# Kernel tuning notes

Hardware: AMD Instinct MI355X
Metric: run time of the kernel (lower is better)

Reference implementation:

```python
import jax, jax.numpy as jnp
import numpy as np

NU, NV, NF = 100000, 50000, 5000
D = 64
S, EUV = 5, 500000
EUF, EVF, EFU, EFV = 1000000, 500000, 1000000, 500000


def _spmm(rows, cols, vals, x, n_out):
    # COO sparse @ dense: out[r] += v * x[c]
    return jax.ops.segment_sum(vals[:, None] * x[cols], rows, num_segments=n_out)


def setup_inputs() -> dict:
    key = jax.random.key(0)
    ks = iter(jax.random.split(key, 32))
    f32 = jnp.float32
    inp = {
        'x_u': jax.random.normal(next(ks), (NU, D), f32),
        'x_v': jax.random.normal(next(ks), (NV, D), f32),
        'x_f': jax.random.normal(next(ks), (NF, D), f32),
    }
    for w in ['W_u_uv', 'W_v_uv', 'W_f2u', 'W_f2v', 'W_u2f', 'W_v2f']:
        inp[w] = jax.random.normal(next(ks), (D, D), f32) * (1.0 / np.sqrt(D))
    def edges(name, shape, n_row, n_col):
        inp[name + '_rows'] = jax.random.randint(next(ks), shape, 0, n_row, jnp.int32)
        inp[name + '_cols'] = jax.random.randint(next(ks), shape, 0, n_col, jnp.int32)
        inp[name + '_vals'] = jax.random.uniform(next(ks), shape, f32)
    edges('uv', (S, EUV), NU, NV)
    edges('vu', (S, EUV), NV, NU)
    edges('uf', (EUF,), NU, NF)
    edges('vf', (EVF,), NV, NF)
    edges('fu', (EFU,), NF, NU)
    edges('fv', (EFV,), NF, NV)
    return inp


def reference(x_u, x_v, x_f, W_u_uv, W_v_uv, W_f2u, W_f2v, W_u2f, W_v2f,
              uv_rows, uv_cols, uv_vals, vu_rows, vu_cols, vu_vals,
              uf_rows, uf_cols, uf_vals, vf_rows, vf_cols, vf_vals,
              fu_rows, fu_cols, fu_vals, fv_rows, fv_cols, fv_vals):
    nu, nv, nf = x_u.shape[0], x_v.shape[0], x_f.shape[0]
    # dense feature transforms (dropout=0 -> identity)
    u2f = x_u @ W_u2f
    v2f = x_v @ W_v2f
    f2u = x_f @ W_f2u
    f2v = x_f @ W_f2v
    tmp_u = x_u @ W_u_uv
    tmp_v = x_v @ W_v_uv
    # sum over rating supports == one segment_sum over flattened edges
    msg_u = _spmm(uv_rows.reshape(-1), uv_cols.reshape(-1), uv_vals.reshape(-1), tmp_v, nu)
    msg_v = _spmm(vu_rows.reshape(-1), vu_cols.reshape(-1), vu_vals.reshape(-1), tmp_u, nv)
    msg_u = msg_u + _spmm(uf_rows, uf_cols, uf_vals, f2u, nu)
    msg_v = msg_v + _spmm(vf_rows, vf_cols, vf_vals, f2v, nv)
    msg_f = _spmm(fu_rows, fu_cols, fu_vals, u2f, nf) + _spmm(fv_rows, fv_cols, fv_vals, v2f, nf)
    return jax.nn.relu(msg_u), jax.nn.relu(msg_v), jax.nn.relu(msg_f)
```

## Files before the change

### kernel.cpp

```cpp
#include <hip/hip_runtime.h>


#define TDIM 64
#define EPB  4096

struct Rel {
    const int* rows; const int* cols; const float* vals;
    int n, chunk0, boff, shift, srcflag, eoff;
};
struct RelPack { Rel r[6]; };

struct TPack {
    const float* X[3]; const float* W1[3]; const float* W2[3];
    unsigned short* Y1[3]; unsigned short* Y2[3];
    int N[3]; int c0[3];
};

struct FSPack {
    int c0A[3], cntA[3], offA[3];
    int c0B[3], cntB[3], offB[3];
};

struct GatherPack {
    const unsigned* srcA[3]; const unsigned* srcB[3];
    int n0, n1;
};

__device__ __forceinline__ unsigned short f2bf(float f) {
    union { float f; unsigned u; } c; c.f = f;
    unsigned r = c.u + 0x7FFFu + ((c.u >> 16) & 1u);
    return (unsigned short)(r >> 16);
}
__device__ __forceinline__ float bflo(unsigned x) { return __uint_as_float(x << 16); }
__device__ __forceinline__ float bfhi(unsigned x) { return __uint_as_float(x & 0xFFFF0000u); }
__device__ __forceinline__ float pval(unsigned p) {
    return __uint_as_float((p & 0x7FFFu) << 16);
}

__global__ __launch_bounds__(256) void transform_fused_kernel(TPack T)
{
    __shared__ float xsT[64 * 68];
    __shared__ float w1s[64 * 64];
    __shared__ float w2s[64 * 64];

    int t = 0;
    if ((int)blockIdx.x >= T.c0[1]) t = 1;
    if ((int)blockIdx.x >= T.c0[2]) t = 2;
    const float* __restrict__ X  = T.X[t];
    const float* __restrict__ W1 = T.W1[t];
    const float* __restrict__ W2 = T.W2[t];
    unsigned short* __restrict__ Y1 = T.Y1[t];
    unsigned short* __restrict__ Y2 = T.Y2[t];
    const int N    = T.N[t];
    const int row0 = (blockIdx.x - T.c0[t]) * 64;
    const int tid  = threadIdx.x;

    for (int i = tid * 4; i < 4096; i += 256 * 4) {
        *(float4*)&w1s[i] = *(const float4*)&W1[i];
        *(float4*)&w2s[i] = *(const float4*)&W2[i];
    }
    {
        const int r  = tid >> 2;
        const int c0 = (tid & 3) * 16;
        const int gr = row0 + r;
        #pragma unroll
        for (int cc = 0; cc < 16; cc += 4) {
            const int c = c0 + cc;
            float4 v = make_float4(0.f, 0.f, 0.f, 0.f);
            if (gr < N) v = *(const float4*)&X[(size_t)gr * TDIM + c];
            xsT[(c + 0) * 68 + r] = v.x;
            xsT[(c + 1) * 68 + r] = v.y;
            xsT[(c + 2) * 68 + r] = v.z;
            xsT[(c + 3) * 68 + r] = v.w;
        }
    }
    __syncthreads();

    const int tx = tid & 15;
    const int ty = tid >> 4;
    float a1[4][4] = {{0.f}}, a2[4][4] = {{0.f}};

    #pragma unroll 8
    for (int k = 0; k < 64; ++k) {
        const float4 xv = *(const float4*)&xsT[k * 68 + ty * 4];
        const float4 w1 = *(const float4*)&w1s[k * 64 + tx * 4];
        const float4 w2 = *(const float4*)&w2s[k * 64 + tx * 4];
        const float xr[4] = {xv.x, xv.y, xv.z, xv.w};
        const float c1[4] = {w1.x, w1.y, w1.z, w1.w};
        const float c2[4] = {w2.x, w2.y, w2.z, w2.w};
        #pragma unroll
        for (int r = 0; r < 4; ++r)
            #pragma unroll
            for (int c = 0; c < 4; ++c) {
                a1[r][c] = fmaf(xr[r], c1[c], a1[r][c]);
                a2[r][c] = fmaf(xr[r], c2[c], a2[r][c]);
            }
    }
    #pragma unroll
    for (int r = 0; r < 4; ++r) {
        const int gr = row0 + ty * 4 + r;
        if (gr < N) {
            ushort4 o1, o2;
            o1.x = f2bf(a1[r][0]); o1.y = f2bf(a1[r][1]);
            o1.z = f2bf(a1[r][2]); o1.w = f2bf(a1[r][3]);
            o2.x = f2bf(a2[r][0]); o2.y = f2bf(a2[r][1]);
            o2.z = f2bf(a2[r][2]); o2.w = f2bf(a2[r][3]);
            ((ushort4*)Y1)[(size_t)gr * 16 + tx] = o1;
            ((ushort4*)Y2)[(size_t)gr * 16 + tx] = o2;
        }
    }
}

__device__ __forceinline__ int find_rel(const RelPack& P, int chunk) {
    int ri = 0;
    if (chunk >= P.r[1].chunk0) ri = 1;
    if (chunk >= P.r[2].chunk0) ri = 2;
    if (chunk >= P.r[3].chunk0) ri = 3;
    if (chunk >= P.r[4].chunk0) ri = 4;
    if (chunk >= P.r[5].chunk0) ri = 5;
    return ri;
}

__global__ __launch_bounds__(512) void bucketize_cm_kernel(
    RelPack P, uint2* __restrict__ recs, int* __restrict__ localStart,
    int* __restrict__ bucketTotal, int NB)
{
    __shared__ int cnt[1024];
    __shared__ int sh[512];
    __shared__ uint2 stage[EPB];

    const int tid   = threadIdx.x;
    const int chunk = blockIdx.x;
    for (int t = tid; t < NB; t += 512) cnt[t] = 0;
    __syncthreads();

    const int ri = find_rel(P, chunk);
    const Rel M = P.r[ri];
    const int i0    = (chunk - M.chunk0) * EPB;
    const int rbase = M.eoff + i0;
    const int count = min(EPB, M.n - i0);

    const unsigned flag = (unsigned)M.srcflag << 31;
    const int mask = (1 << M.shift) - 1;

    int      m_[EPB / 512];
    unsigned x_[EPB / 512];
    #pragma unroll
    for (int k = 0; k < EPB / 512; ++k) {
        const int i = i0 + tid + k * 512;
        m_[k] = -1;
        if (i < M.n) {
            const int row = M.rows[i];
            const int b   = M.boff + (row >> M.shift);
            m_[k] = (b << 8) | (row & mask);
            x_[k] = (unsigned)M.cols[i] | flag;
            atomicAdd(&cnt[b], 1);
        }
    }
    __syncthreads();

    const int i0b = 2 * tid, i1b = 2 * tid + 1;
    const int v0 = (i0b < NB) ? cnt[i0b] : 0;
    const int v1 = (i1b < NB) ? cnt[i1b] : 0;
    if (v0) atomicAdd(&bucketTotal[i0b], v0);
    if (v1) atomicAdd(&bucketTotal[i1b], v1);
    sh[tid] = v0 + v1;
    __syncthreads();
    for (int off = 1; off < 512; off <<= 1) {
        const int x = (tid >= off) ? sh[tid - off] : 0;
        __syncthreads();
        sh[tid] += x;
        __syncthreads();
    }
    const int base0 = tid ? sh[tid - 1] : 0;

    const size_t lb = (size_t)chunk * (NB + 1);
    if (i0b < NB) localStart[lb + i0b] = base0;
    if (i1b < NB) localStart[lb + i1b] = base0 + v0;
    if (i0b == NB)      localStart[lb + NB] = base0;
    else if (i1b == NB) localStart[lb + NB] = base0 + v0;
    if (i0b < NB) cnt[i0b] = base0;
    if (i1b < NB) cnt[i1b] = base0 + v0;
    __syncthreads();

    #pragma unroll
    for (int k = 0; k < EPB / 512; ++k) {
        if (m_[k] >= 0) {
            const int i   = i0 + tid + k * 512;
            const int bin = m_[k] >> 8;
            const int pos = atomicAdd(&cnt[bin], 1);
            uint2 rec;
            rec.x = x_[k];
            rec.y = ((unsigned)(m_[k] & 255) << 16) | (unsigned)f2bf(M.vals[i]);
            stage[pos] = rec;
        }
    }
    __syncthreads();

    #pragma unroll
    for (int k = 0; k < EPB / 512; ++k) {
        const int j = tid + k * 512;
        if (j < count) recs[rbase + j] = stage[j];
    }
}

__global__ __launch_bounds__(256) void bscan_kernel(
    const int* __restrict__ bucketTotal, int* __restrict__ bbase, int NB)
{
    __shared__ int sh[256];
    __shared__ int carry;
    const int t = threadIdx.x;
    if (t == 0) carry = 0;
    __syncthreads();
    for (int b0 = 0; b0 < NB; b0 += 256) {
        const int idx = b0 + t;
        const int c = (idx < NB) ? bucketTotal[idx] : 0;
        sh[t] = c;
        __syncthreads();
        for (int off = 1; off < 256; off <<= 1) {
            const int x = (t >= off) ? sh[t - off] : 0;
            __syncthreads();
            sh[t] += x;
            __syncthreads();
        }
        const int cbase = carry;
        if (idx < NB) bbase[idx] = cbase + sh[t] - c;
        __syncthreads();
        if (t == 0) carry = cbase + sh[255];
        __syncthreads();
    }
    if (t == 0) bbase[NB] = carry;
}

__global__ __launch_bounds__(512) void finesort_kernel(
    const uint2* __restrict__ recs, const int* __restrict__ localStart,
    const int* __restrict__ bbase, FSPack F, int* __restrict__ p2,
    unsigned* __restrict__ arena,
    int nbU, int nbV, int NU, int NV, int NF, int NB, int ntot_rows)
{
    __shared__ int cnt[512];
    __shared__ int sh[512];
    __shared__ int runS[1024], runE[1024];

    const int b   = blockIdx.x;
    const int tid = threadIdx.x;

    int t, lb, rowbase;
    if (b < nbU)              { t = 0; lb = b;              rowbase = 0; }
    else if (b < nbU + nbV)   { t = 1; lb = b - nbU;        rowbase = NU; }
    else                      { t = 2; lb = b - nbU - nbV;  rowbase = NU + NV; }
    const int shift     = (t == 2) ? 6 : 8;
    const int Ntype     = (t == 0) ? NU : (t == 1) ? NV : NF;
    const int row_start = lb << shift;
    const int nrows     = min(1 << shift, Ntype - row_start);
    const int nbins     = (1 << shift) * 2;
    const int grow0     = rowbase + row_start;

    const unsigned addB = (t == 0) ? (unsigned)NV : (t == 1) ? (unsigned)NU : 0u;

    const int nA = F.cntA[t], nB_ = F.cntB[t];
    const int nRuns = nA + nB_;

    for (int i = tid; i < nRuns; i += 512) {
        int c, base;
        if (i < nA) { c = F.c0A[t] + i;        base = F.offA[t] + i * EPB; }
        else        { int k = i - nA;
                      c = F.c0B[t] + k;        base = F.offB[t] + k * EPB; }
        const size_t lbi = (size_t)c * (NB + 1) + b;
        runS[i] = base + localStart[lbi];
        runE[i] = base + localStart[lbi + 1];
    }
    if (tid < nbins) cnt[tid] = 0;
    __syncthreads();

    const int s = bbase[b];
    const int e = bbase[b + 1];
    const int grp = tid >> 4;
    const int gl  = tid & 15;

    for (int ridx = grp; ridx < nRuns; ridx += 32) {
        const int rs = runS[ridx], re = runE[ridx];
        for (int j = rs + gl; j < re; j += 16) {
            const uint2 r = recs[j];
            const int bin = (int)((r.y >> 16) << 1) | (int)(r.x >> 31);
            atomicAdd(&cnt[bin], 1);
        }
    }
    __syncthreads();

    const int v = (tid < nbins) ? cnt[tid] : 0;
    sh[tid] = v;
    __syncthreads();
    for (int off = 1; off < 512; off <<= 1) {
        const int x = (tid >= off) ? sh[tid - off] : 0;
        __syncthreads();
        sh[tid] += x;
        __syncthreads();
    }
    const int excl = sh[tid] - v;
    if (tid < nbins) cnt[tid] = excl;
    if (tid < nrows * 2) p2[2 * grow0 + tid] = s + excl;
    if (b == NB - 1 && tid == 0) p2[2 * ntot_rows] = e;
    __syncthreads();

    for (int ridx = grp; ridx < nRuns; ridx += 32) {
        const int rs = runS[ridx], re = runE[ridx];
        for (int j = rs + gl; j < re; j += 16) {
            const uint2 r = recs[j];
            const int bin = (int)((r.y >> 16) << 1) | (int)(r.x >> 31);
            const int pos = s + atomicAdd(&cnt[bin], 1);
            const unsigned colp = (r.x & 0x7FFFFFFFu)
                                + ((r.x & 0x80000000u) ? addB : 0u);
            arena[pos] = (colp << 15) | (r.y & 0x7FFFu);
        }
    }
}

__device__ __forceinline__ void accum_seg(
    const unsigned* __restrict__ src, const unsigned* __restrict__ arena,
    const int s, const int e, const int g, const int li4,
    float (&acc)[8])
{
    if (s >= e) return;
    const int nb = (e - s + 7) >> 3;
    const unsigned* __restrict__ srcp = src + li4;

    unsigned x0[4], x1[4], x2[4], x3[4];
    float w0, w1, w2, w3;

    auto issue = [&](int j, unsigned* x, float& w) {
        const int idx = j + g;
        const bool ok = idx < e;
        const unsigned cv = arena[ok ? idx : s];
        w = ok ? pval(cv) : 0.f;
        const uint4 xv = *(const uint4*)&srcp[(cv >> 15) * 32u];
        x[0] = xv.x; x[1] = xv.y; x[2] = xv.z; x[3] = xv.w;
    };
    auto fmab = [&](const unsigned* x, float w) {
        #pragma unroll
        for (int q = 0; q < 4; ++q) {
            acc[2 * q]     = fmaf(w, bflo(x[q]), acc[2 * q]);
            acc[2 * q + 1] = fmaf(w, bfhi(x[q]), acc[2 * q + 1]);
        }
    };

    issue(s,      x0, w0);
    issue(s + 8,  x1, w1);
    issue(s + 16, x2, w2);
    issue(s + 24, x3, w3);
    __builtin_amdgcn_sched_barrier(0);

    int k = 0;
    for (;;) {
        fmab(x0, w0);
        if (k + 4 < nb) issue(s + (k + 4) * 8, x0, w0);
        __builtin_amdgcn_sched_barrier(0);
        if (++k >= nb) break;
        fmab(x1, w1);
        if (k + 4 < nb) issue(s + (k + 4) * 8, x1, w1);
        __builtin_amdgcn_sched_barrier(0);
        if (++k >= nb) break;
        fmab(x2, w2);
        if (k + 4 < nb) issue(s + (k + 4) * 8, x2, w2);
        __builtin_amdgcn_sched_barrier(0);
        if (++k >= nb) break;
        fmab(x3, w3);
        if (k + 4 < nb) issue(s + (k + 4) * 8, x3, w3);
        __builtin_amdgcn_sched_barrier(0);
        if (++k >= nb) break;
    }
}

__global__ __launch_bounds__(256) void gather_all_kernel(
    const int* __restrict__ p2, const unsigned* __restrict__ arena,
    GatherPack G, float* __restrict__ out, int nrow_total)
{
    const int gid  = (blockIdx.x * 256 + threadIdx.x) >> 6;
    const int lane = threadIdx.x & 63;
    const int g    = lane >> 3;
    const int li   = lane & 7;
    const int li4  = li * 4;
    if (gid >= nrow_total) return;
    const int wid = nrow_total - 1 - gid;

    int seg = 0;
    if (wid >= G.n1)      seg = 2;
    else if (wid >= G.n0) seg = 1;
    seg = __builtin_amdgcn_readfirstlane(seg);

    const int pa = __builtin_amdgcn_readfirstlane(p2[2 * wid]);
    const int pe = __builtin_amdgcn_readfirstlane(p2[2 * wid + 2]);

    float acc[8];
    #pragma unroll
    for (int k = 0; k < 8; ++k) acc[k] = 0.f;

    if (seg < 2) {
        accum_seg(G.srcA[seg], arena, pa, pe, g, li4, acc);
    } else {
        const int pm = __builtin_amdgcn_readfirstlane(p2[2 * wid + 1]);
        accum_seg(G.srcA[2], arena, pa, pm, g, li4, acc);
        accum_seg(G.srcB[2], arena, pm, pe, g, li4, acc);
    }

    #pragma unroll
    for (int k = 0; k < 8; ++k) {
        acc[k] += __shfl_xor(acc[k], 8, 64);
        acc[k] += __shfl_xor(acc[k], 16, 64);
        acc[k] += __shfl_xor(acc[k], 32, 64);
    }

    if (g == 0) {
        float4 o0, o1;
        o0.x = fmaxf(acc[0], 0.f); o0.y = fmaxf(acc[1], 0.f);
        o0.z = fmaxf(acc[2], 0.f); o0.w = fmaxf(acc[3], 0.f);
        o1.x = fmaxf(acc[4], 0.f); o1.y = fmaxf(acc[5], 0.f);
        o1.z = fmaxf(acc[6], 0.f); o1.w = fmaxf(acc[7], 0.f);
        float4* dst = (float4*)(out + (size_t)wid * 64 + li * 8);
        dst[0] = o0;
        dst[1] = o1;
    }
}

extern "C" void kernel_launch(void* const* d_in, const int* in_sizes, int n_in,
                              void* d_out, int out_size, void* d_ws, size_t ws_size,
                              hipStream_t stream)
{
    const float* x_u    = (const float*)d_in[0];
    const float* x_v    = (const float*)d_in[1];
    const float* x_f    = (const float*)d_in[2];
    const float* W_u_uv = (const float*)d_in[3];
    const float* W_v_uv = (const float*)d_in[4];
    const float* W_f2u  = (const float*)d_in[5];
    const float* W_f2v  = (const float*)d_in[6];
    const float* W_u2f  = (const float*)d_in[7];
    const float* W_v2f  = (const float*)d_in[8];

    const int* rows_[6] = {(const int*)d_in[9],  (const int*)d_in[12],
                           (const int*)d_in[15], (const int*)d_in[18],
                           (const int*)d_in[21], (const int*)d_in[24]};
    const int* cols_[6] = {(const int*)d_in[10], (const int*)d_in[13],
                           (const int*)d_in[16], (const int*)d_in[19],
                           (const int*)d_in[22], (const int*)d_in[25]};
    const float* vals_[6] = {(const float*)d_in[11], (const float*)d_in[14],
                             (const float*)d_in[17], (const float*)d_in[20],
                             (const float*)d_in[23], (const float*)d_in[26]};

    const int NU = in_sizes[0] / TDIM;
    const int NV = in_sizes[1] / TDIM;
    const int NF = in_sizes[2] / TDIM;
    const int E_[6] = {in_sizes[9], in_sizes[12], in_sizes[15],
                       in_sizes[18], in_sizes[21], in_sizes[24]};

    const int nbU = (NU + 255) >> 8;
    const int nbV = (NV + 255) >> 8;
    const int nbF = (NF + 63) >> 6;
    const int NB  = nbU + nbV + nbF;
    const int ntot_rows = NU + NV + NF;

    const int boff_[6]  = {0, nbU, 0, nbU, nbU + nbV, nbU + nbV};
    const int shift_[6] = {8, 8, 8, 8, 6, 6};
    const int sflag_[6] = {0, 0, 1, 1, 0, 1};

    size_t etot = 0;
    int eoff_[6];
    for (int r = 0; r < 6; ++r) { eoff_[r] = (int)etot; etot += (size_t)E_[r]; }

    RelPack P;
    int nchunks = 0;
    int relchunks[6];
    for (int r = 0; r < 6; ++r) {
        P.r[r].rows = rows_[r]; P.r[r].cols = cols_[r]; P.r[r].vals = vals_[r];
        P.r[r].n = E_[r]; P.r[r].chunk0 = nchunks;
        P.r[r].boff = boff_[r]; P.r[r].shift = shift_[r]; P.r[r].srcflag = sflag_[r];
        P.r[r].eoff = eoff_[r];
        relchunks[r] = (E_[r] + EPB - 1) / EPB;
        nchunks += relchunks[r];
    }

    char* wsb = (char*)d_ws;
    size_t o = 0;
    auto alloc = [&](size_t bytes) {
        char* p = wsb + o;
        o = (o + bytes + 15) & ~(size_t)15;
        return p;
    };
    unsigned short* utab = (unsigned short*)alloc(((size_t)NV + NF) * TDIM * 2);
    unsigned short* vtab = (unsigned short*)alloc(((size_t)NU + NF) * TDIM * 2);
    unsigned short* u2f  = (unsigned short*)alloc((size_t)NU * TDIM * 2);
    unsigned short* v2f  = (unsigned short*)alloc((size_t)NV * TDIM * 2);
    unsigned short* tmp_v = utab;
    unsigned short* f2u   = utab + (size_t)NV * TDIM;
    unsigned short* tmp_u = vtab;
    unsigned short* f2v   = vtab + (size_t)NU * TDIM;
    int* localStart  = (int*)alloc((size_t)nchunks * (NB + 1) * 4);
    int* bucketTotal = (int*)alloc((size_t)NB * 4);
    int* bbase       = (int*)alloc((size_t)(NB + 1) * 4);
    int* p2          = (int*)alloc((size_t)(2 * ntot_rows + 1) * 4);
    uint2* recs      = (uint2*)alloc(etot * 8);
    unsigned* arena  = (unsigned*)alloc(etot * 4);
    (void)ws_size;

    TPack T;
    T.X[0] = x_u; T.W1[0] = W_u_uv; T.W2[0] = W_u2f; T.Y1[0] = tmp_u; T.Y2[0] = u2f; T.N[0] = NU;
    T.X[1] = x_v; T.W1[1] = W_v_uv; T.W2[1] = W_v2f; T.Y1[1] = tmp_v; T.Y2[1] = v2f; T.N[1] = NV;
    T.X[2] = x_f; T.W1[2] = W_f2u;  T.W2[2] = W_f2v; T.Y1[2] = f2u;  T.Y2[2] = f2v; T.N[2] = NF;
    T.c0[0] = 0;
    T.c0[1] = (NU + 63) / 64;
    T.c0[2] = T.c0[1] + (NV + 63) / 64;
    const int tchunks = T.c0[2] + (NF + 63) / 64;
    transform_fused_kernel<<<tchunks, 256, 0, stream>>>(T);

    hipMemsetAsync(bucketTotal, 0, (size_t)NB * sizeof(int), stream);
    bucketize_cm_kernel<<<nchunks, 512, 0, stream>>>(P, recs, localStart, bucketTotal, NB);
    bscan_kernel<<<1, 256, 0, stream>>>(bucketTotal, bbase, NB);

    FSPack F;
    const int Arel[3] = {0, 1, 4}, Brel[3] = {2, 3, 5};
    for (int t = 0; t < 3; ++t) {
        F.c0A[t] = P.r[Arel[t]].chunk0; F.cntA[t] = relchunks[Arel[t]]; F.offA[t] = eoff_[Arel[t]];
        F.c0B[t] = P.r[Brel[t]].chunk0; F.cntB[t] = relchunks[Brel[t]]; F.offB[t] = eoff_[Brel[t]];
    }
    finesort_kernel<<<NB, 512, 0, stream>>>(
        recs, localStart, bbase, F, p2, arena, nbU, nbV, NU, NV, NF, NB, ntot_rows);

    GatherPack G;
    G.srcA[0] = (const unsigned*)utab;  G.srcB[0] = (const unsigned*)utab;
    G.srcA[1] = (const unsigned*)vtab;  G.srcB[1] = (const unsigned*)vtab;
    G.srcA[2] = (const unsigned*)u2f;   G.srcB[2] = (const unsigned*)v2f;
    G.n0 = NU; G.n1 = NU + NV;

    gather_all_kernel<<<(ntot_rows + 3) / 4, 256, 0, stream>>>(
        p2, arena, G, (float*)d_out, ntot_rows);
}
```

Before: 489.6 us.

## Split sort records into final payload and byte bin arrays; halve bucket width

The bucketize kernel now writes the final packed payload (column with source offset, plus truncated bf16 value) and a separate one-byte bin index, replacing the 8-byte record. The finesort pass then reads one byte per edge for counting and copies the payload word directly, cutting intermediate memory traffic and per-edge ALU work. Buckets for user and item rows shrink from 256 to 128 rows, which roughly doubles the bucket count (up to 1280). That gives more finesort blocks for parallelism but makes the localStart table larger and adds more per-chunk scan work.

```diff
diff --git a/kernel.cpp b/kernel.cpp
--- a/kernel.cpp
+++ b/kernel.cpp
@@ -6,7 +6,7 @@
 
 struct Rel {
     const int* rows; const int* cols; const float* vals;
-    int n, chunk0, boff, shift, srcflag, eoff;
+    int n, chunk0, boff, shift, srcflag, eoff, coladd;
 };
 struct RelPack { Rel r[6]; };
 
@@ -122,12 +122,13 @@
 }
 
 __global__ __launch_bounds__(512) void bucketize_cm_kernel(
-    RelPack P, uint2* __restrict__ recs, int* __restrict__ localStart,
-    int* __restrict__ bucketTotal, int NB)
-{
-    __shared__ int cnt[1024];
+    RelPack P, unsigned* __restrict__ pay, unsigned char* __restrict__ binb,
+    int* __restrict__ localStart, int* __restrict__ bucketTotal, int NB)
+{
+    __shared__ int cnt[1280];
     __shared__ int sh[512];
-    __shared__ uint2 stage[EPB];
+    __shared__ unsigned stage_pay[EPB];
+    __shared__ unsigned char stage_bin[EPB];
 
     const int tid   = threadIdx.x;
     const int chunk = blockIdx.x;
@@ -140,8 +141,8 @@
     const int rbase = M.eoff + i0;
     const int count = min(EPB, M.n - i0);
 
-    const unsigned flag = (unsigned)M.srcflag << 31;
     const int mask = (1 << M.shift) - 1;
+    const unsigned sf = (unsigned)M.srcflag;
 
     int      m_[EPB / 512];
     unsigned x_[EPB / 512];
@@ -153,18 +154,20 @@
             const int row = M.rows[i];
             const int b   = M.boff + (row >> M.shift);
             m_[k] = (b << 8) | (row & mask);
-            x_[k] = (unsigned)M.cols[i] | flag;
+            x_[k] = (unsigned)M.cols[i] + (unsigned)M.coladd;
             atomicAdd(&cnt[b], 1);
         }
     }
     __syncthreads();
 
-    const int i0b = 2 * tid, i1b = 2 * tid + 1;
-    const int v0 = (i0b < NB) ? cnt[i0b] : 0;
-    const int v1 = (i1b < NB) ? cnt[i1b] : 0;
-    if (v0) atomicAdd(&bucketTotal[i0b], v0);
-    if (v1) atomicAdd(&bucketTotal[i1b], v1);
-    sh[tid] = v0 + v1;
+    int myv[3]; int lsum = 0;
+    #pragma unroll
+    for (int j = 0; j < 3; ++j) {
+        const int idx = tid * 3 + j;
+        myv[j] = (idx < NB) ? cnt[idx] : 0;
+        lsum += myv[j];
+    }
+    sh[tid] = lsum;
     __syncthreads();
     for (int off = 1; off < 512; off <<= 1) {
         const int x = (tid >= off) ? sh[tid - off] : 0;
@@ -172,27 +175,30 @@
         sh[tid] += x;
         __syncthreads();
     }
-    const int base0 = tid ? sh[tid - 1] : 0;
-
+    int prefix = tid ? sh[tid - 1] : 0;
     const size_t lb = (size_t)chunk * (NB + 1);
-    if (i0b < NB) localStart[lb + i0b] = base0;
-    if (i1b < NB) localStart[lb + i1b] = base0 + v0;
-    if (i0b == NB)      localStart[lb + NB] = base0;
-    else if (i1b == NB) localStart[lb + NB] = base0 + v0;
-    if (i0b < NB) cnt[i0b] = base0;
-    if (i1b < NB) cnt[i1b] = base0 + v0;
+    #pragma unroll
+    for (int j = 0; j < 3; ++j) {
+        const int idx = tid * 3 + j;
+        if (idx < NB) {
+            localStart[lb + idx] = prefix;
+            if (myv[j]) atomicAdd(&bucketTotal[idx], myv[j]);
+            cnt[idx] = prefix;
+        } else if (idx == NB) {
+            localStart[lb + NB] = prefix;
+        }
+        prefix += myv[j];
+    }
     __syncthreads();
 
     #pragma unroll
     for (int k = 0; k < EPB / 512; ++k) {
         if (m_[k] >= 0) {
             const int i   = i0 + tid + k * 512;
-            const int bin = m_[k] >> 8;
-            const int pos = atomicAdd(&cnt[bin], 1);
-            uint2 rec;
-            rec.x = x_[k];
-            rec.y = ((unsigned)(m_[k] & 255) << 16) | (unsigned)f2bf(M.vals[i]);
-            stage[pos] = rec;
+            const int b   = m_[k] >> 8;
+            const int pos = atomicAdd(&cnt[b], 1);
+            stage_pay[pos] = (x_[k] << 15) | ((unsigned)f2bf(M.vals[i]) & 0x7FFFu);
+            stage_bin[pos] = (unsigned char)(((m_[k] & 255) << 1) | sf);
         }
     }
     __syncthreads();
@@ -200,7 +206,14 @@
     #pragma unroll
     for (int k = 0; k < EPB / 512; ++k) {
         const int j = tid + k * 512;
-        if (j < count) recs[rbase + j] = stage[j];
+        if (j < count) pay[rbase + j] = stage_pay[j];
+    }
+    {
+        const int nfull = count >> 2;
+        unsigned* bout = (unsigned*)(binb + rbase);
+        const unsigned* bsrc = (const unsigned*)stage_bin;
+        for (int j = tid; j < nfull; j += 512) bout[j] = bsrc[j];
+        if (tid < (count & 3)) binb[rbase + nfull * 4 + tid] = stage_bin[nfull * 4 + tid];
     }
 }
 
@@ -233,9 +246,9 @@
 }
 
 __global__ __launch_bounds__(512) void finesort_kernel(
-    const uint2* __restrict__ recs, const int* __restrict__ localStart,
-    const int* __restrict__ bbase, FSPack F, int* __restrict__ p2,
-    unsigned* __restrict__ arena,
+    const unsigned* __restrict__ pay, const unsigned char* __restrict__ binb,
+    const int* __restrict__ localStart, const int* __restrict__ bbase,
+    FSPack F, int* __restrict__ p2, unsigned* __restrict__ arena,
     int nbU, int nbV, int NU, int NV, int NF, int NB, int ntot_rows)
 {
     __shared__ int cnt[512];
@@ -249,14 +262,12 @@
     if (b < nbU)              { t = 0; lb = b;              rowbase = 0; }
     else if (b < nbU + nbV)   { t = 1; lb = b - nbU;        rowbase = NU; }
     else                      { t = 2; lb = b - nbU - nbV;  rowbase = NU + NV; }
-    const int shift     = (t == 2) ? 6 : 8;
+    const int shift     = (t == 2) ? 6 : 7;
     const int Ntype     = (t == 0) ? NU : (t == 1) ? NV : NF;
     const int row_start = lb << shift;
     const int nrows     = min(1 << shift, Ntype - row_start);
     const int nbins     = (1 << shift) * 2;
     const int grow0     = rowbase + row_start;
-
-    const unsigned addB = (t == 0) ? (unsigned)NV : (t == 1) ? (unsigned)NU : 0u;
 
     const int nA = F.cntA[t], nB_ = F.cntB[t];
     const int nRuns = nA + nB_;
@@ -281,9 +292,7 @@
     for (int ridx = grp; ridx < nRuns; ridx += 32) {
         const int rs = runS[ridx], re = runE[ridx];
         for (int j = rs + gl; j < re; j += 16) {
-            const uint2 r = recs[j];
-            const int bin = (int)((r.y >> 16) << 1) | (int)(r.x >> 31);
-            atomicAdd(&cnt[bin], 1);
+            atomicAdd(&cnt[binb[j]], 1);
         }
     }
     __syncthreads();
@@ -306,12 +315,9 @@
     for (int ridx = grp; ridx < nRuns; ridx += 32) {
         const int rs = runS[ridx], re = runE[ridx];
         for (int j = rs + gl; j < re; j += 16) {
-            const uint2 r = recs[j];
-            const int bin = (int)((r.y >> 16) << 1) | (int)(r.x >> 31);
+            const int bin = binb[j];
             const int pos = s + atomicAdd(&cnt[bin], 1);
-            const unsigned colp = (r.x & 0x7FFFFFFFu)
-                                + ((r.x & 0x80000000u) ? addB : 0u);
-            arena[pos] = (colp << 15) | (r.y & 0x7FFFu);
+            arena[pos] = pay[j];
         }
     }
 }
@@ -452,15 +458,16 @@
     const int E_[6] = {in_sizes[9], in_sizes[12], in_sizes[15],
                        in_sizes[18], in_sizes[21], in_sizes[24]};
 
-    const int nbU = (NU + 255) >> 8;
-    const int nbV = (NV + 255) >> 8;
+    const int nbU = (NU + 127) >> 7;
+    const int nbV = (NV + 127) >> 7;
     const int nbF = (NF + 63) >> 6;
     const int NB  = nbU + nbV + nbF;
     const int ntot_rows = NU + NV + NF;
 
-    const int boff_[6]  = {0, nbU, 0, nbU, nbU + nbV, nbU + nbV};
-    const int shift_[6] = {8, 8, 8, 8, 6, 6};
-    const int sflag_[6] = {0, 0, 1, 1, 0, 1};
+    const int boff_[6]   = {0, nbU, 0, nbU, nbU + nbV, nbU + nbV};
+    const int shift_[6]  = {7, 7, 7, 7, 6, 6};
+    const int sflag_[6]  = {0, 0, 1, 1, 0, 1};
+    const int coladd_[6] = {0, 0, NV, NU, 0, 0};
 
     size_t etot = 0;
     int eoff_[6];
@@ -473,7 +480,7 @@
         P.r[r].rows = rows_[r]; P.r[r].cols = cols_[r]; P.r[r].vals = vals_[r];
         P.r[r].n = E_[r]; P.r[r].chunk0 = nchunks;
         P.r[r].boff = boff_[r]; P.r[r].shift = shift_[r]; P.r[r].srcflag = sflag_[r];
-        P.r[r].eoff = eoff_[r];
+        P.r[r].eoff = eoff_[r]; P.r[r].coladd = coladd_[r];
         relchunks[r] = (E_[r] + EPB - 1) / EPB;
         nchunks += relchunks[r];
     }
@@ -497,8 +504,9 @@
     int* bucketTotal = (int*)alloc((size_t)NB * 4);
     int* bbase       = (int*)alloc((size_t)(NB + 1) * 4);
     int* p2          = (int*)alloc((size_t)(2 * ntot_rows + 1) * 4);
-    uint2* recs      = (uint2*)alloc(etot * 8);
-    unsigned* arena  = (unsigned*)alloc(etot * 4);
+    unsigned* pay        = (unsigned*)alloc(etot * 4);
+    unsigned char* binb  = (unsigned char*)alloc(etot);
+    unsigned* arena      = (unsigned*)alloc(etot * 4);
     (void)ws_size;
 
     TPack T;
@@ -512,7 +520,7 @@
     transform_fused_kernel<<<tchunks, 256, 0, stream>>>(T);
 
     hipMemsetAsync(bucketTotal, 0, (size_t)NB * sizeof(int), stream);
-    bucketize_cm_kernel<<<nchunks, 512, 0, stream>>>(P, recs, localStart, bucketTotal, NB);
+    bucketize_cm_kernel<<<nchunks, 512, 0, stream>>>(P, pay, binb, localStart, bucketTotal, NB);
     bscan_kernel<<<1, 256, 0, stream>>>(bucketTotal, bbase, NB);
 
     FSPack F;
@@ -522,7 +530,7 @@
         F.c0B[t] = P.r[Brel[t]].chunk0; F.cntB[t] = relchunks[Brel[t]]; F.offB[t] = eoff_[Brel[t]];
     }
     finesort_kernel<<<NB, 512, 0, stream>>>(
-        recs, localStart, bbase, F, p2, arena, nbU, nbV, NU, NV, NF, NB, ntot_rows);
+        pay, binb, localStart, bbase, F, p2, arena, nbU, nbV, NU, NV, NF, NB, ntot_rows);
 
     GatherPack G;
     G.srcA[0] = (const unsigned*)utab;  G.srcB[0] = (const unsigned*)utab;
```

Result: slower. 524.5 us (+7.1%).
